# Kernel optimization log

Hardware: AMD Instinct MI355X
Metric: run time of the kernel (lower is better)

## Reference

```python
import jax, jax.numpy as jnp
import numpy as np

# Sparse grid constants (closed over; coords live on this grid)
B, H, W = 2, 640, 640
N = 409600
CIN, CH, COUT = 64, 64, 64
K = 3
PAD = (K - 1) // 2


def setup_inputs() -> dict:
    key = jax.random.key(0)
    ks = jax.random.split(key, 6)
    # unique active coordinates via permutation of the dense grid
    lin = jax.random.permutation(ks[0], B * H * W)[:N]
    b = lin // (H * W)
    rem = lin % (H * W)
    coords = jnp.stack([b, rem // W, rem % W], axis=1).astype(jnp.int32)  # [N,3]
    features = jax.random.normal(ks[1], (N, CIN), jnp.float32)
    w1 = jax.random.normal(ks[2], (K, K, CIN, CH), jnp.float32) * (1.0 / np.sqrt(K * K * CIN))
    b1 = jnp.zeros((CH,), jnp.float32)
    w2 = jax.random.normal(ks[3], (K, K, CH, COUT), jnp.float32) * (1.0 / np.sqrt(K * K * CH))
    b2 = jnp.zeros((COUT,), jnp.float32)
    wd = jax.random.normal(ks[4], (CIN, COUT), jnp.float32) * (1.0 / np.sqrt(CIN))
    return {"features": features, "coords": coords, "w1": w1, "b1": b1,
            "w2": w2, "b2": b2, "wd": wd}


def _build_grid(coords):
    # dense hash: grid[b,y,x] = row index into features, -1 if inactive
    grid = jnp.full((B, H, W), -1, dtype=jnp.int32)
    return grid.at[coords[:, 0], coords[:, 1], coords[:, 2]].set(
        jnp.arange(N, dtype=jnp.int32))


def _subm_conv(feat, coords, grid, w, bias):
    # Submanifold conv: out only at active sites; gather-matmul-accumulate per offset.
    cb, cy, cx = coords[:, 0], coords[:, 1], coords[:, 2]
    out = jnp.zeros((N, w.shape[-1]), feat.dtype)
    for ky in range(K):              # small fixed kernel loop (rulebook offsets)
        for kx in range(K):
            dy, dx = ky - PAD, kx - PAD
            ny, nx = cy + dy, cx + dx
            inb = (ny >= 0) & (ny < H) & (nx >= 0) & (nx < W)
            nidx = grid[cb, jnp.clip(ny, 0, H - 1), jnp.clip(nx, 0, W - 1)]
            valid = inb & (nidx >= 0)
            g = feat[jnp.where(valid, nidx, 0)]          # [N, Cin] gather
            g = jnp.where(valid[:, None], g, 0.0)
            out = out + g @ w[ky, kx]                    # per-offset GEMM
    if bias is not None:
        out = out + bias
    return out


def reference(features, coords, w1, b1, w2, b2, wd):
    grid = _build_grid(coords)
    out = jax.nn.relu(_subm_conv(features, coords, grid, w1, b1))
    out = jax.nn.relu(_subm_conv(out, coords, grid, w2, b2))
    residual = features @ wd                  # 1x1 subm conv, no bias
    out = jax.nn.relu(out + residual)         # sparse_add: identical index sets
    return out
```

## Files before the change

kernel.cpp:

```cpp
#include <hip/hip_runtime.h>
#include <hip/hip_bf16.h>
#include <stdint.h>

#define NP 409600
#define HG 640
#define WG 640
#define HW (HG*WG)
#define TPB  40
#define NTILE 3200

typedef __bf16 bf16x8 __attribute__((ext_vector_type(8)));
typedef float f32x4 __attribute__((ext_vector_type(4)));


__global__ void hist_kernel(const int* __restrict__ coords, int* __restrict__ hist) {
    int i = blockIdx.x * 256 + threadIdx.x;
    int b = coords[3*i], y = coords[3*i+1], x = coords[3*i+2];
    atomicAdd(&hist[b*(TPB*TPB) + (y>>4)*TPB + (x>>4)], 1);
}

__global__ void scan_kernel(int* __restrict__ hist) {
    __shared__ int part[256];
    int t = threadIdx.x;
    int loc[13];
    int s = 0;
    #pragma unroll
    for (int k = 0; k < 13; ++k) {
        int idx = t*13 + k;
        int v = (idx < NTILE) ? hist[idx] : 0;
        loc[k] = s; s += v;
    }
    part[t] = s;
    __syncthreads();
    for (int off = 1; off < 256; off <<= 1) {
        int v = (t >= off) ? part[t - off] : 0;
        __syncthreads();
        part[t] += v;
        __syncthreads();
    }
    int pre = (t > 0) ? part[t-1] : 0;
    #pragma unroll
    for (int k = 0; k < 13; ++k) {
        int idx = t*13 + k;
        if (idx < NTILE) hist[idx] = pre + loc[k];
    }
}

__global__ void ord_kernel(const int* __restrict__ coords, int* __restrict__ offs,
                           int* __restrict__ ord, int* __restrict__ lsort) {
    int i = blockIdx.x * 256 + threadIdx.x;
    int b = coords[3*i], y = coords[3*i+1], x = coords[3*i+2];
    int tile = b*(TPB*TPB) + (y>>4)*TPB + (x>>4);
    int pos = atomicAdd(&offs[tile], 1);
    ord[pos]   = i;
    lsort[pos] = b*HW + y*WG + x;
}

__global__ void scatter_sorted_kernel(const int* __restrict__ lsort, int* __restrict__ grid) {
    int j = blockIdx.x * 256 + threadIdx.x;
    grid[lsort[j]] = j;
}

__global__ void perm_cast_kernel(const float* __restrict__ f, const int* __restrict__ ord,
                                 __hip_bfloat16* __restrict__ fpermb) {
    int t = blockIdx.x * 256 + threadIdx.x;
    int j = t >> 3, part = t & 7;
    int i = ord[j];
    const float4* p = (const float4*)(f + (long)i*64 + part*8);
    float4 a = p[0], b = p[1];
    union { uint4 q; __hip_bfloat16 h[8]; } u;
    u.h[0] = __float2bfloat16(a.x); u.h[1] = __float2bfloat16(a.y);
    u.h[2] = __float2bfloat16(a.z); u.h[3] = __float2bfloat16(a.w);
    u.h[4] = __float2bfloat16(b.x); u.h[5] = __float2bfloat16(b.y);
    u.h[6] = __float2bfloat16(b.z); u.h[7] = __float2bfloat16(b.w);
    *(uint4*)(fpermb + (long)j*64 + part*8) = u.q;
}

__global__ void nbr_kernel(const int* __restrict__ lsort, const int* __restrict__ grid,
                           int* __restrict__ nbrp) {
    int j = blockIdx.x * 256 + threadIdx.x;
    int lin = lsort[j];
    int b = lin / HW;
    int rem = lin - b*HW;
    int y = rem / WG;
    int x = rem - y*WG;
    int baseg = b*HW;
    #pragma unroll
    for (int tt = 0; tt < 9; ++tt) {
        if (tt == 4) continue;
        int ti = tt < 4 ? tt : tt - 1;
        int ny = y + tt/3 - 1, nx = x + tt%3 - 1;
        int g = -1;
        if (ny >= 0 && ny < HG && nx >= 0 && nx < WG)
            g = grid[baseg + ny*WG + nx];
        nbrp[ti*NP + j] = g;
    }
}

__global__ void cast_w_kernel(const float* __restrict__ w1, const float* __restrict__ w2,
                              const float* __restrict__ wd,
                              __hip_bfloat16* __restrict__ wc1, __hip_bfloat16* __restrict__ wc2) {
    int i = blockIdx.x * 256 + threadIdx.x;
    if (i < 9*4096) {
        int t = i >> 12, r = i & 4095, n = r >> 6, k = r & 63;
        wc1[i] = __float2bfloat16(w1[(t << 12) + (k << 6) + n]);
    }
    int j = i - 9*4096;
    if (j >= 0 && j < 10*4096) {
        int t = j >> 12, r = j & 4095, n = r >> 6, k = r & 63;
        float v = (t < 9) ? w2[(t << 12) + (k << 6) + n] : wd[(k << 6) + n];
        wc2[j] = __float2bfloat16(v);
    }
}


#define LDA 72
#define LDB 72

template<bool FINAL>
__launch_bounds__(256)
__global__ void conv_kernel(const __hip_bfloat16* __restrict__ src,
                            const __hip_bfloat16* __restrict__ idsrc,
                            const int* __restrict__ nbrp,
                            const int* __restrict__ ord,
                            const __hip_bfloat16* __restrict__ wT,
                            const float* __restrict__ bias,
                            __hip_bfloat16* __restrict__ out_bf,
                            float* __restrict__ out_f) {
    __shared__ __align__(16) __hip_bfloat16 As[128 * LDA];
    __shared__ __align__(16) __hip_bfloat16 Bs[64 * LDB];

    const int tid = threadIdx.x;
    const int sbid = (blockIdx.x & 7) * 400 + (blockIdx.x >> 3);
    const int base = sbid * 128;
    const int wave = tid >> 6, lane = tid & 63;
    const int srow = tid >> 1, shalf = tid & 1;

    f32x4 acc[2][4];
    f32x4 accR[2][4];
    #pragma unroll
    for (int i = 0; i < 2; ++i)
        #pragma unroll
        for (int j = 0; j < 4; ++j) {
            acc[i][j]  = (f32x4){0.f, 0.f, 0.f, 0.f};
            accR[i][j] = (f32x4){0.f, 0.f, 0.f, 0.f};
        }

    const int NT = FINAL ? 10 : 9;

    auto gpos = [&](int t) -> int {
        if (t == 4) return base + srow;
        int ti = t < 4 ? t : t - 1;
        return nbrp[ti*NP + base + srow];
    };

    auto do_mfma = [&](f32x4 (&ac)[2][4]) {
        #pragma unroll
        for (int ks = 0; ks < 2; ++ks) {
            int kb = ks*32 + (lane >> 4)*8;
            bf16x8 a0 = *(const bf16x8*)(As + (wave*32      + (lane & 15))*LDA + kb);
            bf16x8 a1 = *(const bf16x8*)(As + (wave*32 + 16 + (lane & 15))*LDA + kb);
            bf16x8 b0 = *(const bf16x8*)(Bs + ( 0 + (lane & 15))*LDB + kb);
            bf16x8 b1 = *(const bf16x8*)(Bs + (16 + (lane & 15))*LDB + kb);
            bf16x8 b2 = *(const bf16x8*)(Bs + (32 + (lane & 15))*LDB + kb);
            bf16x8 b3 = *(const bf16x8*)(Bs + (48 + (lane & 15))*LDB + kb);
            ac[0][0] = __builtin_amdgcn_mfma_f32_16x16x32_bf16(a0, b0, ac[0][0], 0, 0, 0);
            ac[0][1] = __builtin_amdgcn_mfma_f32_16x16x32_bf16(a0, b1, ac[0][1], 0, 0, 0);
            ac[0][2] = __builtin_amdgcn_mfma_f32_16x16x32_bf16(a0, b2, ac[0][2], 0, 0, 0);
            ac[0][3] = __builtin_amdgcn_mfma_f32_16x16x32_bf16(a0, b3, ac[0][3], 0, 0, 0);
            ac[1][0] = __builtin_amdgcn_mfma_f32_16x16x32_bf16(a1, b0, ac[1][0], 0, 0, 0);
            ac[1][1] = __builtin_amdgcn_mfma_f32_16x16x32_bf16(a1, b1, ac[1][1], 0, 0, 0);
            ac[1][2] = __builtin_amdgcn_mfma_f32_16x16x32_bf16(a1, b2, ac[1][2], 0, 0, 0);
            ac[1][3] = __builtin_amdgcn_mfma_f32_16x16x32_bf16(a1, b3, ac[1][3], 0, 0, 0);
        }
    };

    int g = gpos(0);

    for (int t = 0; t < NT; ++t) {
        if (t) __syncthreads();

        const __hip_bfloat16* sp = (FINAL && t == NT - 1) ? idsrc : src;
        uint4 v0, v1, v2, v3;
        if (g >= 0) {
            const uint4* p = (const uint4*)(sp + (long)g*64 + shalf*32);
            v0 = p[0]; v1 = p[1]; v2 = p[2]; v3 = p[3];
        } else {
            v0 = v1 = v2 = v3 = make_uint4(0u, 0u, 0u, 0u);
        }
        uint4* dst = (uint4*)(As + srow*LDA + shalf*32);
        dst[0] = v0; dst[1] = v1; dst[2] = v2; dst[3] = v3;

        const uint4* wp = (const uint4*)(wT + t*4096);
        #pragma unroll
        for (int jj = 0; jj < 2; ++jj) {
            int e = tid + jj*256;
            int l = e * 8;
            int n = l >> 6, k = l & 63;
            *(uint4*)(Bs + n*LDB + k) = wp[e];
        }
        __syncthreads();

        if (t + 1 < NT)
            g = (FINAL && t + 1 == NT - 1) ? (base + srow) : gpos(t + 1);

        if (FINAL && t == NT - 1) do_mfma(accR);
        else                      do_mfma(acc);
    }

    const int col = lane & 15, quad = lane >> 4;
    #pragma unroll
    for (int cb = 0; cb < 4; ++cb) {
        float bv = bias[cb*16 + col];
        #pragma unroll
        for (int mb = 0; mb < 2; ++mb) {
            #pragma unroll
            for (int r = 0; r < 4; ++r) {
                float v = acc[mb][cb][r] + bv;
                v = v > 0.f ? v : 0.f;
                int srt = base + wave*32 + mb*16 + quad*4 + r;
                int c   = cb*16 + col;
                if (FINAL) {
                    v += accR[mb][cb][r];
                    v = v > 0.f ? v : 0.f;
                    long row = ord[srt];
                    out_f[row*64 + c] = v;
                } else {
                    out_bf[(long)srt*64 + c] = __float2bfloat16(v);
                }
            }
        }
    }
}


extern "C" void kernel_launch(void* const* d_in, const int* in_sizes, int n_in,
                              void* d_out, int out_size, void* d_ws, size_t ws_size,
                              hipStream_t stream) {
    const float* features = (const float*)d_in[0];
    const int*   coords   = (const int*)d_in[1];
    const float* w1 = (const float*)d_in[2];
    const float* b1 = (const float*)d_in[3];
    const float* w2 = (const float*)d_in[4];
    const float* b2 = (const float*)d_in[5];
    const float* wd = (const float*)d_in[6];
    float* out = (float*)d_out;

    char* ws = (char*)d_ws;
    int*            grid   = (int*)ws;
    int*            nbrp   = (int*)(ws + 3276800);
    int*            ord    = (int*)(ws + 16384000);
    __hip_bfloat16* fpermb = (__hip_bfloat16*)(ws + 18022400);
    __hip_bfloat16* y1     = (__hip_bfloat16*)(ws + 70451200);
    __hip_bfloat16* wc1    = (__hip_bfloat16*)(ws + 122880000);
    __hip_bfloat16* wc2    = (__hip_bfloat16*)(ws + 122953728);
    int* lsort = (int*)(ws + 70451200);
    int* hist  = (int*)(ws + 70451200 + 1638400);

    hipMemsetAsync(grid, 0xFF, (size_t)HW * 2 * sizeof(int), stream);
    hipMemsetAsync(hist, 0x00, (size_t)NTILE * sizeof(int), stream);

    hist_kernel          <<<1600,  256, 0, stream>>>(coords, hist);
    scan_kernel          <<<1,     256, 0, stream>>>(hist);
    ord_kernel           <<<1600,  256, 0, stream>>>(coords, hist, ord, lsort);
    cast_w_kernel        <<<304,   256, 0, stream>>>(w1, w2, wd, wc1, wc2);
    scatter_sorted_kernel<<<1600,  256, 0, stream>>>(lsort, grid);
    nbr_kernel           <<<1600,  256, 0, stream>>>(lsort, grid, nbrp);
    perm_cast_kernel     <<<12800, 256, 0, stream>>>(features, ord, fpermb);

    conv_kernel<false><<<3200, 256, 0, stream>>>(fpermb, nullptr, nbrp, ord, wc1, b1, y1, nullptr);
    conv_kernel<true ><<<3200, 256, 0, stream>>>(y1, fpermb, nbrp, ord, wc2, b2, nullptr, out);
}
```

Measured before the change: 422.2 us.

## Load conv operands directly into MFMA registers and fuse grid scatter into ord

After: 620.6 us. +47.0%, slower.

```diff
diff --git a/kernel.cpp b/kernel.cpp
--- a/kernel.cpp
+++ b/kernel.cpp
@@ -47,18 +47,16 @@
 }
 
 __global__ void ord_kernel(const int* __restrict__ coords, int* __restrict__ offs,
-                           int* __restrict__ ord, int* __restrict__ lsort) {
+                           int* __restrict__ ord, int* __restrict__ lsort,
+                           int* __restrict__ grid) {
     int i = blockIdx.x * 256 + threadIdx.x;
     int b = coords[3*i], y = coords[3*i+1], x = coords[3*i+2];
     int tile = b*(TPB*TPB) + (y>>4)*TPB + (x>>4);
     int pos = atomicAdd(&offs[tile], 1);
+    int lin = b*HW + y*WG + x;
     ord[pos]   = i;
-    lsort[pos] = b*HW + y*WG + x;
-}
-
-__global__ void scatter_sorted_kernel(const int* __restrict__ lsort, int* __restrict__ grid) {
-    int j = blockIdx.x * 256 + threadIdx.x;
-    grid[lsort[j]] = j;
+    lsort[pos] = lin;
+    grid[lin]  = pos;
 }
 
 __global__ void perm_cast_kernel(const float* __restrict__ f, const int* __restrict__ ord,
@@ -114,9 +112,6 @@
 }
 
 
-#define LDA 72
-#define LDB 72
-
 template<bool FINAL>
 __launch_bounds__(256)
 __global__ void conv_kernel(const __hip_bfloat16* __restrict__ src,
@@ -127,106 +122,128 @@
                             const float* __restrict__ bias,
                             __hip_bfloat16* __restrict__ out_bf,
                             float* __restrict__ out_f) {
-    __shared__ __align__(16) __hip_bfloat16 As[128 * LDA];
-    __shared__ __align__(16) __hip_bfloat16 Bs[64 * LDB];
-
     const int tid = threadIdx.x;
     const int sbid = (blockIdx.x & 7) * 400 + (blockIdx.x >> 3);
     const int base = sbid * 128;
     const int wave = tid >> 6, lane = tid & 63;
-    const int srow = tid >> 1, shalf = tid & 1;
+    const int mrow = lane & 15;
+    const int kq   = lane >> 4;
+    const int r0 = base + wave*32 + mrow;
+    const int r1 = r0 + 16;
+
+    union { uint4 q; bf16x8 v; } uz; uz.q = make_uint4(0u,0u,0u,0u);
+    const bf16x8 Z = uz.v;
+
+    auto ldA = [&](const __hip_bfloat16* p, int g, int kb) -> bf16x8 {
+        union { uint4 q; bf16x8 v; } u;
+        u.q = *(const uint4*)(p + (long)g*64 + kb);
+        return u.v;
+    };
 
     f32x4 acc[2][4];
-    f32x4 accR[2][4];
     #pragma unroll
     for (int i = 0; i < 2; ++i)
         #pragma unroll
-        for (int j = 0; j < 4; ++j) {
-            acc[i][j]  = (f32x4){0.f, 0.f, 0.f, 0.f};
-            accR[i][j] = (f32x4){0.f, 0.f, 0.f, 0.f};
-        }
-
-    const int NT = FINAL ? 10 : 9;
-
-    auto gpos = [&](int t) -> int {
-        if (t == 4) return base + srow;
-        int ti = t < 4 ? t : t - 1;
-        return nbrp[ti*NP + base + srow];
-    };
-
-    auto do_mfma = [&](f32x4 (&ac)[2][4]) {
+        for (int j = 0; j < 4; ++j)
+            acc[i][j] = (f32x4){0.f, 0.f, 0.f, 0.f};
+
+    int g0 = nbrp[r0];
+    int g1 = nbrp[r1];
+
+    #pragma unroll
+    for (int t = 0; t < 9; ++t) {
+        const __hip_bfloat16* wp = wT + t*4096;
+        const int kb0 = kq*8, kb1 = 32 + kq*8;
+        bf16x8 a00 = (g0 >= 0) ? ldA(src, g0, kb0) : Z;
+        bf16x8 a01 = (g0 >= 0) ? ldA(src, g0, kb1) : Z;
+        bf16x8 a10 = (g1 >= 0) ? ldA(src, g1, kb0) : Z;
+        bf16x8 a11 = (g1 >= 0) ? ldA(src, g1, kb1) : Z;
+        if (t + 1 < 9) {
+            int tn = t + 1;
+            if (tn == 4) { g0 = r0; g1 = r1; }
+            else {
+                int ti = tn < 4 ? tn : tn - 1;
+                g0 = nbrp[ti*NP + r0];
+                g1 = nbrp[ti*NP + r1];
+            }
+        }
         #pragma unroll
         for (int ks = 0; ks < 2; ++ks) {
-            int kb = ks*32 + (lane >> 4)*8;
-            bf16x8 a0 = *(const bf16x8*)(As + (wave*32      + (lane & 15))*LDA + kb);
-            bf16x8 a1 = *(const bf16x8*)(As + (wave*32 + 16 + (lane & 15))*LDA + kb);
-            bf16x8 b0 = *(const bf16x8*)(Bs + ( 0 + (lane & 15))*LDB + kb);
-            bf16x8 b1 = *(const bf16x8*)(Bs + (16 + (lane & 15))*LDB + kb);
-            bf16x8 b2 = *(const bf16x8*)(Bs + (32 + (lane & 15))*LDB + kb);
-            bf16x8 b3 = *(const bf16x8*)(Bs + (48 + (lane & 15))*LDB + kb);
-            ac[0][0] = __builtin_amdgcn_mfma_f32_16x16x32_bf16(a0, b0, ac[0][0], 0, 0, 0);
-            ac[0][1] = __builtin_amdgcn_mfma_f32_16x16x32_bf16(a0, b1, ac[0][1], 0, 0, 0);
-            ac[0][2] = __builtin_amdgcn_mfma_f32_16x16x32_bf16(a0, b2, ac[0][2], 0, 0, 0);
-            ac[0][3] = __builtin_amdgcn_mfma_f32_16x16x32_bf16(a0, b3, ac[0][3], 0, 0, 0);
-            ac[1][0] = __builtin_amdgcn_mfma_f32_16x16x32_bf16(a1, b0, ac[1][0], 0, 0, 0);
-            ac[1][1] = __builtin_amdgcn_mfma_f32_16x16x32_bf16(a1, b1, ac[1][1], 0, 0, 0);
-            ac[1][2] = __builtin_amdgcn_mfma_f32_16x16x32_bf16(a1, b2, ac[1][2], 0, 0, 0);
-            ac[1][3] = __builtin_amdgcn_mfma_f32_16x16x32_bf16(a1, b3, ac[1][3], 0, 0, 0);
-        }
-    };
-
-    int g = gpos(0);
-
-    for (int t = 0; t < NT; ++t) {
-        if (t) __syncthreads();
-
-        const __hip_bfloat16* sp = (FINAL && t == NT - 1) ? idsrc : src;
-        uint4 v0, v1, v2, v3;
-        if (g >= 0) {
-            const uint4* p = (const uint4*)(sp + (long)g*64 + shalf*32);
-            v0 = p[0]; v1 = p[1]; v2 = p[2]; v3 = p[3];
-        } else {
-            v0 = v1 = v2 = v3 = make_uint4(0u, 0u, 0u, 0u);
-        }
-        uint4* dst = (uint4*)(As + srow*LDA + shalf*32);
-        dst[0] = v0; dst[1] = v1; dst[2] = v2; dst[3] = v3;
-
-        const uint4* wp = (const uint4*)(wT + t*4096);
-        #pragma unroll
-        for (int jj = 0; jj < 2; ++jj) {
-            int e = tid + jj*256;
-            int l = e * 8;
-            int n = l >> 6, k = l & 63;
-            *(uint4*)(Bs + n*LDB + k) = wp[e];
-        }
-        __syncthreads();
-
-        if (t + 1 < NT)
-            g = (FINAL && t + 1 == NT - 1) ? (base + srow) : gpos(t + 1);
-
-        if (FINAL && t == NT - 1) do_mfma(accR);
-        else                      do_mfma(acc);
-    }
-
-    const int col = lane & 15, quad = lane >> 4;
-    #pragma unroll
-    for (int cb = 0; cb < 4; ++cb) {
-        float bv = bias[cb*16 + col];
-        #pragma unroll
-        for (int mb = 0; mb < 2; ++mb) {
+            int kb = ks*32 + kq*8;
+            bf16x8 b0 = *(const bf16x8*)(wp + ( 0 + mrow)*64 + kb);
+            bf16x8 b1 = *(const bf16x8*)(wp + (16 + mrow)*64 + kb);
+            bf16x8 b2 = *(const bf16x8*)(wp + (32 + mrow)*64 + kb);
+            bf16x8 b3 = *(const bf16x8*)(wp + (48 + mrow)*64 + kb);
+            bf16x8 a0 = ks ? a01 : a00;
+            bf16x8 a1 = ks ? a11 : a10;
+            acc[0][0] = __builtin_amdgcn_mfma_f32_16x16x32_bf16(a0, b0, acc[0][0], 0, 0, 0);
+            acc[0][1] = __builtin_amdgcn_mfma_f32_16x16x32_bf16(a0, b1, acc[0][1], 0, 0, 0);
+            acc[0][2] = __builtin_amdgcn_mfma_f32_16x16x32_bf16(a0, b2, acc[0][2], 0, 0, 0);
+            acc[0][3] = __builtin_amdgcn_mfma_f32_16x16x32_bf16(a0, b3, acc[0][3], 0, 0, 0);
+            acc[1][0] = __builtin_amdgcn_mfma_f32_16x16x32_bf16(a1, b0, acc[1][0], 0, 0, 0);
+            acc[1][1] = __builtin_amdgcn_mfma_f32_16x16x32_bf16(a1, b1, acc[1][1], 0, 0, 0);
+            acc[1][2] = __builtin_amdgcn_mfma_f32_16x16x32_bf16(a1, b2, acc[1][2], 0, 0, 0);
+            acc[1][3] = __builtin_amdgcn_mfma_f32_16x16x32_bf16(a1, b3, acc[1][3], 0, 0, 0);
+        }
+    }
+
+    const int col = mrow, quad = kq;
+
+    if (FINAL) {
+        f32x4 accR[2][4];
+        #pragma unroll
+        for (int i = 0; i < 2; ++i)
             #pragma unroll
-            for (int r = 0; r < 4; ++r) {
-                float v = acc[mb][cb][r] + bv;
-                v = v > 0.f ? v : 0.f;
-                int srt = base + wave*32 + mb*16 + quad*4 + r;
-                int c   = cb*16 + col;
-                if (FINAL) {
+            for (int j = 0; j < 4; ++j)
+                accR[i][j] = (f32x4){0.f, 0.f, 0.f, 0.f};
+        const __hip_bfloat16* wp = wT + 9*4096;
+        #pragma unroll
+        for (int ks = 0; ks < 2; ++ks) {
+            int kb = ks*32 + kq*8;
+            bf16x8 a0 = ldA(idsrc, r0, kb);
+            bf16x8 a1 = ldA(idsrc, r1, kb);
+            bf16x8 b0 = *(const bf16x8*)(wp + ( 0 + mrow)*64 + kb);
+            bf16x8 b1 = *(const bf16x8*)(wp + (16 + mrow)*64 + kb);
+            bf16x8 b2 = *(const bf16x8*)(wp + (32 + mrow)*64 + kb);
+            bf16x8 b3 = *(const bf16x8*)(wp + (48 + mrow)*64 + kb);
+            accR[0][0] = __builtin_amdgcn_mfma_f32_16x16x32_bf16(a0, b0, accR[0][0], 0, 0, 0);
+            accR[0][1] = __builtin_amdgcn_mfma_f32_16x16x32_bf16(a0, b1, accR[0][1], 0, 0, 0);
+            accR[0][2] = __builtin_amdgcn_mfma_f32_16x16x32_bf16(a0, b2, accR[0][2], 0, 0, 0);
+            accR[0][3] = __builtin_amdgcn_mfma_f32_16x16x32_bf16(a0, b3, accR[0][3], 0, 0, 0);
+            accR[1][0] = __builtin_amdgcn_mfma_f32_16x16x32_bf16(a1, b0, accR[1][0], 0, 0, 0);
+            accR[1][1] = __builtin_amdgcn_mfma_f32_16x16x32_bf16(a1, b1, accR[1][1], 0, 0, 0);
+            accR[1][2] = __builtin_amdgcn_mfma_f32_16x16x32_bf16(a1, b2, accR[1][2], 0, 0, 0);
+            accR[1][3] = __builtin_amdgcn_mfma_f32_16x16x32_bf16(a1, b3, accR[1][3], 0, 0, 0);
+        }
+        #pragma unroll
+        for (int cb = 0; cb < 4; ++cb) {
+            float bv = bias[cb*16 + col];
+            #pragma unroll
+            for (int mb = 0; mb < 2; ++mb) {
+                #pragma unroll
+                for (int r = 0; r < 4; ++r) {
+                    float v = acc[mb][cb][r] + bv;
+                    v = v > 0.f ? v : 0.f;
                     v += accR[mb][cb][r];
                     v = v > 0.f ? v : 0.f;
+                    int srt = base + wave*32 + mb*16 + quad*4 + r;
                     long row = ord[srt];
-                    out_f[row*64 + c] = v;
-                } else {
-                    out_bf[(long)srt*64 + c] = __float2bfloat16(v);
+                    out_f[row*64 + cb*16 + col] = v;
+                }
+            }
+        }
+    } else {
+        #pragma unroll
+        for (int cb = 0; cb < 4; ++cb) {
+            float bv = bias[cb*16 + col];
+            #pragma unroll
+            for (int mb = 0; mb < 2; ++mb) {
+                #pragma unroll
+                for (int r = 0; r < 4; ++r) {
+                    float v = acc[mb][cb][r] + bv;
+                    v = v > 0.f ? v : 0.f;
+                    int srt = base + wave*32 + mb*16 + quad*4 + r;
+                    out_bf[(long)srt*64 + cb*16 + col] = __float2bfloat16(v);
                 }
             }
         }
@@ -260,13 +277,12 @@
     hipMemsetAsync(grid, 0xFF, (size_t)HW * 2 * sizeof(int), stream);
     hipMemsetAsync(hist, 0x00, (size_t)NTILE * sizeof(int), stream);
 
-    hist_kernel          <<<1600,  256, 0, stream>>>(coords, hist);
-    scan_kernel          <<<1,     256, 0, stream>>>(hist);
-    ord_kernel           <<<1600,  256, 0, stream>>>(coords, hist, ord, lsort);
-    cast_w_kernel        <<<304,   256, 0, stream>>>(w1, w2, wd, wc1, wc2);
-    scatter_sorted_kernel<<<1600,  256, 0, stream>>>(lsort, grid);
-    nbr_kernel           <<<1600,  256, 0, stream>>>(lsort, grid, nbrp);
-    perm_cast_kernel     <<<12800, 256, 0, stream>>>(features, ord, fpermb);
+    hist_kernel     <<<1600,  256, 0, stream>>>(coords, hist);
+    scan_kernel     <<<1,     256, 0, stream>>>(hist);
+    ord_kernel      <<<1600,  256, 0, stream>>>(coords, hist, ord, lsort, grid);
+    cast_w_kernel   <<<304,   256, 0, stream>>>(w1, w2, wd, wc1, wc2);
+    nbr_kernel      <<<1600,  256, 0, stream>>>(lsort, grid, nbrp);
+    perm_cast_kernel<<<12800, 256, 0, stream>>>(features, ord, fpermb);
 
     conv_kernel<false><<<3200, 256, 0, stream>>>(fpermb, nullptr, nbrp, ord, wc1, b1, y1, nullptr);
     conv_kernel<true ><<<3200, 256, 0, stream>>>(y1, fpermb, nbrp, ord, wc2, b2, nullptr, out);
```

## Double-buffer gather tiles, read pre-swizzled weights from global, fuse grid scatter

Applied to the files above, without the earlier changes.

New measurement: 625.1 us. 48.1% more time.

```diff
diff --git a/kernel.cpp b/kernel.cpp
--- a/kernel.cpp
+++ b/kernel.cpp
@@ -47,25 +47,24 @@
 }
 
 __global__ void ord_kernel(const int* __restrict__ coords, int* __restrict__ offs,
-                           int* __restrict__ ord, int* __restrict__ lsort) {
+                           int* __restrict__ ord, int* __restrict__ lsort,
+                           int* __restrict__ grid, int* __restrict__ inv) {
     int i = blockIdx.x * 256 + threadIdx.x;
     int b = coords[3*i], y = coords[3*i+1], x = coords[3*i+2];
     int tile = b*(TPB*TPB) + (y>>4)*TPB + (x>>4);
     int pos = atomicAdd(&offs[tile], 1);
+    int lin = b*HW + y*WG + x;
     ord[pos]   = i;
-    lsort[pos] = b*HW + y*WG + x;
-}
-
-__global__ void scatter_sorted_kernel(const int* __restrict__ lsort, int* __restrict__ grid) {
-    int j = blockIdx.x * 256 + threadIdx.x;
-    grid[lsort[j]] = j;
-}
-
-__global__ void perm_cast_kernel(const float* __restrict__ f, const int* __restrict__ ord,
+    lsort[pos] = lin;
+    grid[lin]  = pos;
+    inv[i]     = pos;
+}
+
+__global__ void perm_cast_kernel(const float* __restrict__ f, const int* __restrict__ inv,
                                  __hip_bfloat16* __restrict__ fpermb) {
     int t = blockIdx.x * 256 + threadIdx.x;
-    int j = t >> 3, part = t & 7;
-    int i = ord[j];
+    int i = t >> 3, part = t & 7;
+    int j = inv[i];
     const float4* p = (const float4*)(f + (long)i*64 + part*8);
     float4 a = p[0], b = p[1];
     union { uint4 q; __hip_bfloat16 h[8]; } u;
@@ -102,20 +101,23 @@
                               __hip_bfloat16* __restrict__ wc1, __hip_bfloat16* __restrict__ wc2) {
     int i = blockIdx.x * 256 + threadIdx.x;
     if (i < 9*4096) {
-        int t = i >> 12, r = i & 4095, n = r >> 6, k = r & 63;
-        wc1[i] = __float2bfloat16(w1[(t << 12) + (k << 6) + n]);
+        int o = i;
+        int e = o & 7, l = (o >> 3) & 63, c = (o >> 9) & 3, ks = (o >> 11) & 1, t = o >> 12;
+        int n = c*16 + (l & 15), k = ks*32 + (l >> 4)*8 + e;
+        wc1[o] = __float2bfloat16(w1[t*4096 + k*64 + n]);
     }
     int j = i - 9*4096;
     if (j >= 0 && j < 10*4096) {
-        int t = j >> 12, r = j & 4095, n = r >> 6, k = r & 63;
-        float v = (t < 9) ? w2[(t << 12) + (k << 6) + n] : wd[(k << 6) + n];
-        wc2[j] = __float2bfloat16(v);
+        int o = j;
+        int e = o & 7, l = (o >> 3) & 63, c = (o >> 9) & 3, ks = (o >> 11) & 1, t = o >> 12;
+        int n = c*16 + (l & 15), k = ks*32 + (l >> 4)*8 + e;
+        float v = (t < 9) ? w2[t*4096 + k*64 + n] : wd[k*64 + n];
+        wc2[o] = __float2bfloat16(v);
     }
 }
 
 
 #define LDA 72
-#define LDB 72
 
 template<bool FINAL>
 __launch_bounds__(256)
@@ -127,43 +129,60 @@
                             const float* __restrict__ bias,
                             __hip_bfloat16* __restrict__ out_bf,
                             float* __restrict__ out_f) {
-    __shared__ __align__(16) __hip_bfloat16 As[128 * LDA];
-    __shared__ __align__(16) __hip_bfloat16 Bs[64 * LDB];
+    __shared__ __align__(16) __hip_bfloat16 As[2][128 * LDA];
 
     const int tid = threadIdx.x;
     const int sbid = (blockIdx.x & 7) * 400 + (blockIdx.x >> 3);
     const int base = sbid * 128;
     const int wave = tid >> 6, lane = tid & 63;
+    const int mrow = lane & 15, kq = lane >> 4;
     const int srow = tid >> 1, shalf = tid & 1;
+
+    const bf16x8* wfrag = (const bf16x8*)wT;
 
     f32x4 acc[2][4];
     f32x4 accR[2][4];
     #pragma unroll
     for (int i = 0; i < 2; ++i)
         #pragma unroll
-        for (int j = 0; j < 4; ++j) {
-            acc[i][j]  = (f32x4){0.f, 0.f, 0.f, 0.f};
-            accR[i][j] = (f32x4){0.f, 0.f, 0.f, 0.f};
-        }
+        for (int j = 0; j < 4; ++j)
+            acc[i][j] = (f32x4){0.f, 0.f, 0.f, 0.f};
 
     const int NT = FINAL ? 10 : 9;
 
     auto gpos = [&](int t) -> int {
         if (t == 4) return base + srow;
+        if (FINAL && t == 9) return base + srow;
         int ti = t < 4 ? t : t - 1;
         return nbrp[ti*NP + base + srow];
     };
 
-    auto do_mfma = [&](f32x4 (&ac)[2][4]) {
+    uint4 v0, v1, v2, v3;
+    auto loadA = [&](int t, int g) {
+        const __hip_bfloat16* sp = (FINAL && t == 9) ? idsrc : src;
+        if (g >= 0) {
+            const uint4* p = (const uint4*)(sp + (long)g*64 + shalf*32);
+            v0 = p[0]; v1 = p[1]; v2 = p[2]; v3 = p[3];
+        } else {
+            v0 = v1 = v2 = v3 = make_uint4(0u, 0u, 0u, 0u);
+        }
+    };
+    auto writeA = [&](int bsel) {
+        uint4* dst = (uint4*)(As[bsel] + srow*LDA + shalf*32);
+        dst[0] = v0; dst[1] = v1; dst[2] = v2; dst[3] = v3;
+    };
+
+    auto mfma_tap = [&](f32x4 (&ac)[2][4], int t, int cur) {
         #pragma unroll
         for (int ks = 0; ks < 2; ++ks) {
-            int kb = ks*32 + (lane >> 4)*8;
-            bf16x8 a0 = *(const bf16x8*)(As + (wave*32      + (lane & 15))*LDA + kb);
-            bf16x8 a1 = *(const bf16x8*)(As + (wave*32 + 16 + (lane & 15))*LDA + kb);
-            bf16x8 b0 = *(const bf16x8*)(Bs + ( 0 + (lane & 15))*LDB + kb);
-            bf16x8 b1 = *(const bf16x8*)(Bs + (16 + (lane & 15))*LDB + kb);
-            bf16x8 b2 = *(const bf16x8*)(Bs + (32 + (lane & 15))*LDB + kb);
-            bf16x8 b3 = *(const bf16x8*)(Bs + (48 + (lane & 15))*LDB + kb);
+            int kb = ks*32 + kq*8;
+            bf16x8 a0 = *(const bf16x8*)(&As[cur][(wave*32      + mrow)*LDA + kb]);
+            bf16x8 a1 = *(const bf16x8*)(&As[cur][(wave*32 + 16 + mrow)*LDA + kb]);
+            int fb = ((t*2 + ks)*4)*64 + lane;
+            bf16x8 b0 = wfrag[fb];
+            bf16x8 b1 = wfrag[fb + 64];
+            bf16x8 b2 = wfrag[fb + 128];
+            bf16x8 b3 = wfrag[fb + 192];
             ac[0][0] = __builtin_amdgcn_mfma_f32_16x16x32_bf16(a0, b0, ac[0][0], 0, 0, 0);
             ac[0][1] = __builtin_amdgcn_mfma_f32_16x16x32_bf16(a0, b1, ac[0][1], 0, 0, 0);
             ac[0][2] = __builtin_amdgcn_mfma_f32_16x16x32_bf16(a0, b2, ac[0][2], 0, 0, 0);
@@ -176,39 +195,31 @@
     };
 
     int g = gpos(0);
-
+    loadA(0, g);
+    writeA(0);
+    g = gpos(1);
+
+    #pragma unroll
     for (int t = 0; t < NT; ++t) {
-        if (t) __syncthreads();
-
-        const __hip_bfloat16* sp = (FINAL && t == NT - 1) ? idsrc : src;
-        uint4 v0, v1, v2, v3;
-        if (g >= 0) {
-            const uint4* p = (const uint4*)(sp + (long)g*64 + shalf*32);
-            v0 = p[0]; v1 = p[1]; v2 = p[2]; v3 = p[3];
+        if (t + 1 < NT) {
+            loadA(t + 1, g);
+            if (t + 2 < NT) g = gpos(t + 2);
+        }
+        __syncthreads();
+        if (FINAL && t == NT - 1) {
+            #pragma unroll
+            for (int i = 0; i < 2; ++i)
+                #pragma unroll
+                for (int j = 0; j < 4; ++j)
+                    accR[i][j] = (f32x4){0.f, 0.f, 0.f, 0.f};
+            mfma_tap(accR, t, t & 1);
         } else {
-            v0 = v1 = v2 = v3 = make_uint4(0u, 0u, 0u, 0u);
-        }
-        uint4* dst = (uint4*)(As + srow*LDA + shalf*32);
-        dst[0] = v0; dst[1] = v1; dst[2] = v2; dst[3] = v3;
-
-        const uint4* wp = (const uint4*)(wT + t*4096);
-        #pragma unroll
-        for (int jj = 0; jj < 2; ++jj) {
-            int e = tid + jj*256;
-            int l = e * 8;
-            int n = l >> 6, k = l & 63;
-            *(uint4*)(Bs + n*LDB + k) = wp[e];
-        }
-        __syncthreads();
-
-        if (t + 1 < NT)
-            g = (FINAL && t + 1 == NT - 1) ? (base + srow) : gpos(t + 1);
-
-        if (FINAL && t == NT - 1) do_mfma(accR);
-        else                      do_mfma(acc);
-    }
-
-    const int col = lane & 15, quad = lane >> 4;
+            mfma_tap(acc, t, t & 1);
+        }
+        if (t + 1 < NT) writeA((t + 1) & 1);
+    }
+
+    const int col = mrow, quad = kq;
     #pragma unroll
     for (int cb = 0; cb < 4; ++cb) {
         float bv = bias[cb*16 + col];
@@ -256,17 +267,17 @@
     __hip_bfloat16* wc2    = (__hip_bfloat16*)(ws + 122953728);
     int* lsort = (int*)(ws + 70451200);
     int* hist  = (int*)(ws + 70451200 + 1638400);
+    int* inv   = (int*)(ws + 70451200 + 1651200);
 
     hipMemsetAsync(grid, 0xFF, (size_t)HW * 2 * sizeof(int), stream);
     hipMemsetAsync(hist, 0x00, (size_t)NTILE * sizeof(int), stream);
 
-    hist_kernel          <<<1600,  256, 0, stream>>>(coords, hist);
-    scan_kernel          <<<1,     256, 0, stream>>>(hist);
-    ord_kernel           <<<1600,  256, 0, stream>>>(coords, hist, ord, lsort);
-    cast_w_kernel        <<<304,   256, 0, stream>>>(w1, w2, wd, wc1, wc2);
-    scatter_sorted_kernel<<<1600,  256, 0, stream>>>(lsort, grid);
-    nbr_kernel           <<<1600,  256, 0, stream>>>(lsort, grid, nbrp);
-    perm_cast_kernel     <<<12800, 256, 0, stream>>>(features, ord, fpermb);
+    hist_kernel     <<<1600,  256, 0, stream>>>(coords, hist);
+    scan_kernel     <<<1,     256, 0, stream>>>(hist);
+    ord_kernel      <<<1600,  256, 0, stream>>>(coords, hist, ord, lsort, grid, inv);
+    cast_w_kernel   <<<304,   256, 0, stream>>>(w1, w2, wd, wc1, wc2);
+    nbr_kernel      <<<1600,  256, 0, stream>>>(lsort, grid, nbrp);
+    perm_cast_kernel<<<12800, 256, 0, stream>>>(features, inv, fpermb);
 
     conv_kernel<false><<<3200, 256, 0, stream>>>(fpermb, nullptr, nbrp, ord, wc1, b1, y1, nullptr);
     conv_kernel<true ><<<3200, 256, 0, stream>>>(y1, fpermb, nbrp, ord, wc2, b2, nullptr, out);
```
